# Kernel optimization log

Measured on AMD Instinct MI355X. Metric: run time of the kernel, lower is better.

## Reference

```python
import jax, jax.numpy as jnp
import numpy as np

LN_EPS = 1e-5   # torch LayerNorm default
NRM_EPS = 1e-8  # normalizer-state epsilon in mLSTMCell


def setup_inputs() -> dict:
    key = jax.random.key(0)
    ks = jax.random.split(key, 3)
    B, T, H, L, O = 32, 256, 1024, 4, 256
    x = jax.random.normal(ks[0], (B, T, H), dtype=jnp.float32)
    # 6 projections per layer in order (q, k, v, i, f, o); Linear stored as [in, out]
    W = jax.random.normal(ks[1], (L, 6, H, H), dtype=jnp.float32) * 0.02
    b = jnp.zeros((L, 6, H), dtype=jnp.float32)
    ln_g = jnp.ones((L, 6, H), dtype=jnp.float32)
    ln_b = jnp.zeros((L, 6, H), dtype=jnp.float32)
    fc_w = jax.random.normal(ks[2], (H, O), dtype=jnp.float32) * 0.02
    fc_b = jnp.zeros((O,), dtype=jnp.float32)
    return {"x": x, "W": W, "b": b, "ln_g": ln_g, "ln_b": ln_b,
            "fc_w": fc_w, "fc_b": fc_b}


def _layer_norm(z, g, beta):
    # z: [6, B, H]; g, beta: [6, H]
    mu = z.mean(-1, keepdims=True)
    var = z.var(-1, keepdims=True)
    return (z - mu) * jax.lax.rsqrt(var + LN_EPS) * g[:, None, :] + beta[:, None, :]


def _cell(x_in, h_prev, c_prev, n_prev, Wl, bl, gl, betal):
    # x_in: [B, H]; states: [B, H]; Wl: [6, H, H]
    z = jnp.einsum('bh,jhd->jbd', x_in, Wl) + bl[:, None, :]
    z = _layer_norm(z, gl, betal)
    q, k, v, zi, zf, zo = z  # q is computed by the original cell but unused
    i = jnp.exp(zi)
    f = jax.nn.sigmoid(zf)
    o = jax.nn.sigmoid(zo)
    # kv_interaction = outer(k, v); sum over dim=1 == sum(k) * v (same math, no [B,H,H])
    kv_sum = k.sum(-1, keepdims=True) * v
    c = f * c_prev + i * kv_sum
    n = f * n_prev + i * k
    n_hat = n / (jnp.linalg.norm(n, axis=-1, keepdims=True) + NRM_EPS)
    h = o * jnp.tanh(c * n_hat)
    return h, c, n


def _mlstm_forward(x, W, b, ln_g, ln_b, fc_w, fc_b):
    B, T, H = x.shape
    L = W.shape[0]
    h0 = jnp.zeros((L, B, H), x.dtype)
    init = (h0, h0, h0)  # (h, c, n)

    def step(carry, x_t):
        h, c, n = carry
        layer_in = x_t
        hs, cs, ns = [], [], []
        for l in range(L):  # small fixed layer count
            h_l, c_l, n_l = _cell(layer_in, h[l], c[l], n[l],
                                  W[l], b[l], ln_g[l], ln_b[l])
            if l > 0:  # residual connection (use_residual=True)
                h_l = h_l + layer_in
            layer_in = h_l
            hs.append(h_l); cs.append(c_l); ns.append(n_l)
        return (jnp.stack(hs), jnp.stack(cs), jnp.stack(ns)), None

    (h, c, n), _ = jax.lax.scan(step, init, jnp.swapaxes(x, 0, 1))
    # output[-1] == top-layer hidden at the final timestep
    out = h[-1] @ fc_w + fc_b  # [B, O]
    return out, (h, c, n)


def reference(x, W, b, ln_g, ln_b, fc_w, fc_b):
    return _mlstm_forward(x, W, b, ln_g, ln_b, fc_w, fc_b)
```

## Files before the change

kernel.cpp:

```cpp
#include <hip/hip_runtime.h>
#include <hip/hip_bf16.h>
#include <math.h>

#define H 1024
#define B 32
#define T 256
#define L 4
#define O 256
#define SEGLEN 16
#define NSEG (T / SEGLEN)

typedef _Float16 half8 __attribute__((ext_vector_type(8)));
typedef _Float16 half4 __attribute__((ext_vector_type(4)));
typedef float f32x4 __attribute__((ext_vector_type(4)));

#define X_PK_OFF   0
#define HB0_OFF    8388608
#define HB1_OFF    16777216
#define WT2_OFF    25165824
#define Z16_OFF    46137344
#define SEGA_OFF   88080384
#define SEGBC_OFF  89128960
#define SEGBN_OFF  90177536
#define STATS_OFF  91226112
#define CARC_OFF   91422720
#define CARN_OFF   92471296
#define FCP_OFF    93519872

__global__ __launch_bounds__(256) void pack_wx(
    const float* __restrict__ W, const float* __restrict__ x,
    _Float16* __restrict__ Wt2, _Float16* __restrict__ x_pk) {
  __shared__ float shmem[32 * 257];
  if (blockIdx.x < 5120) {
    int tile = blockIdx.x;
    int m_idx = tile >> 8;
    int kt = (tile >> 4) & 15, ntt = tile & 15;
    int l = m_idx / 5, jj = m_idx % 5;
    const float* Wf = W + ((size_t)(l * 6 + jj + 1) << 20);
    _Float16* out = Wt2 + ((size_t)m_idx << 20);
    float (*ts)[65] = (float(*)[65])shmem;
    int k0 = kt * 64, n0 = ntt * 64;
#pragma unroll
    for (int s = 0; s < 16; ++s) {
      int e = threadIdx.x + s * 256;
      int kk = e >> 6, col = e & 63;
      ts[kk][col] = Wf[(size_t)(k0 + kk) * H + n0 + col];
    }
    __syncthreads();
#pragma unroll
    for (int gi = 0; gi < 2; ++gi) {
      int g = threadIdx.x * 2 + gi;
      int l64 = g & 63, ksl = (g >> 6) & 1, ntl = g >> 7;
      int nn = l64 & 15, kh = l64 >> 4;
      half8 tmp;
#pragma unroll
      for (int e = 0; e < 8; ++e)
        tmp[e] = (_Float16)ts[ksl * 32 + kh * 8 + e][ntl * 16 + nn];
      *(half8*)&out[(size_t)((ntt * 4 + ntl) * 32 + kt * 2 + ksl) * 512 +
                    (size_t)l64 * 8] = tmp;
    }
  } else {
    int t = blockIdx.x - 5120;
    float (*ld)[257] = (float(*)[257])shmem;
    for (int c = 0; c < 4; ++c) {
      if (c) __syncthreads();
#pragma unroll
      for (int s = 0; s < 32; ++s) {
        int e2 = threadIdx.x + s * 256;
        int b = e2 >> 8, col = e2 & 255;
        ld[b][col] = x[((size_t)b * T + t) * H + c * 256 + col];
      }
      __syncthreads();
#pragma unroll
      for (int s3 = 0; s3 < 4; ++s3) {
        int gg = threadIdx.x * 4 + s3;
        int l64 = gg & 63, ksl = (gg >> 6) & 7, bt = gg >> 9;
        int nn = l64 & 15, kh = l64 >> 4;
        int b = bt * 16 + nn;
        half8 tmp;
#pragma unroll
        for (int e = 0; e < 8; ++e)
          tmp[e] = (_Float16)ld[b][ksl * 32 + kh * 8 + e];
        *(half8*)&x_pk[(size_t)t * 32768 + (size_t)bt * 16384 +
                       (size_t)(c * 8 + ksl) * 512 + (size_t)l64 * 8] = tmp;
      }
    }
  }
}

__global__ __launch_bounds__(512) void gemm_big(
    const _Float16* __restrict__ A_pk, const _Float16* __restrict__ Wl,
    _Float16* __restrict__ z16) {
  int raw = blockIdx.x;
  int xcd = raw & 7, c = raw >> 3;
  int bm = (xcd >> 1) * 16 + (c & 15);
  int bn = (xcd & 1) * 10 + (c >> 4);
  int w = threadIdx.x >> 6, lane = threadIdx.x & 63;
  int wm = w >> 2, wn = w & 3;

  __shared__ _Float16 smem[24576];

  int j = bn >> 2;
  const _Float16* gsrc[3];
  int ldst[3];
#pragma unroll
  for (int q = 0; q < 3; ++q) {
    int f = w * 3 + q;
    if (f < 8) {
      gsrc[q] = A_pk + (size_t)(bm * 8 + f) * 16384 + lane * 8;
      ldst[q] = f * 512 + lane * 8;
    } else {
      int nf = f - 8;
      gsrc[q] = Wl + ((size_t)j << 20) + (size_t)((bn & 3) * 16 + nf) * 16384 + lane * 8;
      ldst[q] = 4096 + nf * 512 + lane * 8;
    }
  }

  half8 stA[3], stB[3];
#pragma unroll
  for (int q = 0; q < 3; ++q) stA[q] = *(const half8*)(gsrc[q]);
#pragma unroll
  for (int q = 0; q < 3; ++q) *(half8*)&smem[ldst[q]] = stA[q];
#pragma unroll
  for (int q = 0; q < 3; ++q) stA[q] = *(const half8*)(gsrc[q] + 512);
  __syncthreads();

  f32x4 acc[4][4] = {};
  int ardo = wm * 2048 + lane * 8;
  int brdo = 4096 + wn * 2048 + lane * 8;

  for (int ks = 0; ks < 32; ks += 2) {
    {
      if (ks + 2 < 32) {
#pragma unroll
        for (int q = 0; q < 3; ++q)
          stB[q] = *(const half8*)(gsrc[q] + (size_t)(ks + 2) * 512);
      }
      half8 a[4], b[4];
#pragma unroll
      for (int i = 0; i < 4; ++i) a[i] = *(const half8*)&smem[ardo + i * 512];
#pragma unroll
      for (int i = 0; i < 4; ++i) b[i] = *(const half8*)&smem[brdo + i * 512];
#pragma unroll
      for (int i = 0; i < 4; ++i)
#pragma unroll
        for (int jf = 0; jf < 4; ++jf)
          acc[i][jf] = __builtin_amdgcn_mfma_f32_16x16x32_f16(a[i], b[jf], acc[i][jf], 0, 0, 0);
#pragma unroll
      for (int q = 0; q < 3; ++q) *(half8*)&smem[12288 + ldst[q]] = stA[q];
      asm volatile("s_waitcnt lgkmcnt(0)" ::: "memory");
      __builtin_amdgcn_s_barrier();
      __builtin_amdgcn_sched_barrier(0);
    }
    {
      if (ks + 3 < 32) {
#pragma unroll
        for (int q = 0; q < 3; ++q)
          stA[q] = *(const half8*)(gsrc[q] + (size_t)(ks + 3) * 512);
      }
      half8 a[4], b[4];
#pragma unroll
      for (int i = 0; i < 4; ++i) a[i] = *(const half8*)&smem[12288 + ardo + i * 512];
#pragma unroll
      for (int i = 0; i < 4; ++i) b[i] = *(const half8*)&smem[12288 + brdo + i * 512];
#pragma unroll
      for (int i = 0; i < 4; ++i)
#pragma unroll
        for (int jf = 0; jf < 4; ++jf)
          acc[i][jf] = __builtin_amdgcn_mfma_f32_16x16x32_f16(a[i], b[jf], acc[i][jf], 0, 0, 0);
      if (ks + 2 < 32) {
#pragma unroll
        for (int q = 0; q < 3; ++q) *(half8*)&smem[ldst[q]] = stB[q];
        asm volatile("s_waitcnt lgkmcnt(0)" ::: "memory");
        __builtin_amdgcn_s_barrier();
        __builtin_amdgcn_sched_barrier(0);
      }
    }
  }
  __syncthreads();

  _Float16 (*cz)[264] = (_Float16(*)[264])smem;
  int hb0 = (bn & 3) * 256;
  for (int p = 0; p < 2; ++p) {
    if (p) __syncthreads();
    if (wm == p) {
#pragma unroll
      for (int i = 0; i < 4; ++i)
#pragma unroll
        for (int jf = 0; jf < 4; ++jf)
#pragma unroll
          for (int r = 0; r < 4; ++r)
            cz[i * 16 + (lane >> 4) * 4 + r][wn * 64 + jf * 16 + (lane & 15)] =
                (_Float16)acc[i][jf][r];
    }
    __syncthreads();
#pragma unroll
    for (int s = 0; s < 4; ++s) {
      int e = threadIdx.x + s * 512;
      int r = e >> 5, h8 = e & 31;
      int m_local = bm * 128 + p * 64 + r;
      half8 vv = *(const half8*)&cz[r][h8 * 8];
      *(half8*)&z16[((size_t)m_local * 5 + j) * 1024 + hb0 + h8 * 8] = vv;
    }
  }
}

__global__ __launch_bounds__(256) void stats_kernel(
    const _Float16* __restrict__ z16, const float* __restrict__ bias,
    const float* __restrict__ ln_g, const float* __restrict__ ln_b,
    float* __restrict__ stats, int l) {
  int row = blockIdx.x, tid = threadIdx.x;
  int h0 = tid * 4;
  float red[13];
#pragma unroll
  for (int jj = 0; jj < 5; ++jj) {
    half4 z4 = *(const half4*)&z16[((size_t)row * 5 + jj) * 1024 + h0];
    float4 bb = *(const float4*)&bias[(size_t)(l * 6 + 1 + jj) * H + h0];
    float vx = (float)z4[0] + bb.x, vy = (float)z4[1] + bb.y,
          vz = (float)z4[2] + bb.z, vw = (float)z4[3] + bb.w;
    red[jj * 2] = vx + vy + vz + vw;
    red[jj * 2 + 1] = vx * vx + vy * vy + vz * vz + vw * vw;
    if (jj == 0) {
      float4 g = *(const float4*)&ln_g[(size_t)(l * 6 + 1) * H + h0];
      float4 be = *(const float4*)&ln_b[(size_t)(l * 6 + 1) * H + h0];
      red[10] = vx * g.x + vy * g.y + vz * g.z + vw * g.w;
      red[11] = g.x + g.y + g.z + g.w;
      red[12] = be.x + be.y + be.z + be.w;
    }
  }
#pragma unroll
  for (int off = 32; off; off >>= 1)
#pragma unroll
    for (int q = 0; q < 13; ++q) red[q] += __shfl_down(red[q], off);
  __shared__ float sb[4][13];
  if ((tid & 63) == 0) {
#pragma unroll
    for (int q = 0; q < 13; ++q) sb[tid >> 6][q] = red[q];
  }
  __syncthreads();
  if (tid == 0) {
    float st[13];
#pragma unroll
    for (int q = 0; q < 13; ++q) st[q] = sb[0][q] + sb[1][q] + sb[2][q] + sb[3][q];
    float* so = stats + (size_t)row * 12;
#pragma unroll
    for (int jj = 0; jj < 5; ++jj) {
      float mu = st[jj * 2] * (1.0f / H);
      float var = st[jj * 2 + 1] * (1.0f / H) - mu * mu;
      so[jj * 2] = mu;
      so[jj * 2 + 1] = rsqrtf(var + 1e-5f);
    }
    float mu0 = st[0] * (1.0f / H);
    float rs0 = rsqrtf(st[1] * (1.0f / H) - mu0 * mu0 + 1e-5f);
    so[10] = rs0 * (st[10] - mu0 * st[11]) + st[12];
    so[11] = 0.f;
  }
}

__global__ __launch_bounds__(256) void scan_p1agg(
    const _Float16* __restrict__ z16, const float* __restrict__ stats,
    const float* __restrict__ bias, const float* __restrict__ ln_g,
    const float* __restrict__ ln_b, float* __restrict__ segA,
    float* __restrict__ segBc, float* __restrict__ segBn, int l) {
  int idx = blockIdx.x * 256 + threadIdx.x;
  int h = idx & 1023;
  int bs = idx >> 10;
  int b = bs & 31, seg = bs >> 5;

  float bz[4], gg[4], bb[4];
#pragma unroll
  for (int jj = 0; jj < 4; ++jj) {
    bz[jj] = bias[(size_t)(l * 6 + 1 + jj) * H + h];
    gg[jj] = ln_g[(size_t)(l * 6 + 1 + jj) * H + h];
    bb[jj] = ln_b[(size_t)(l * 6 + 1 + jj) * H + h];
  }
  float A = 1.f, bc = 0.f, bn = 0.f;
#pragma unroll 2
  for (int u = 0; u < SEGLEN; ++u) {
    int row = (seg * SEGLEN + u) * 32 + b;
    size_t zb = ((size_t)row * 5) * 1024 + h;
    float zk = (float)z16[zb];
    float zv = (float)z16[zb + 1024];
    float zi = (float)z16[zb + 2048];
    float zf = (float)z16[zb + 3072];
    const float* st = stats + (size_t)row * 12;
    float k   = (zk + bz[0] - st[0]) * st[1] * gg[0] + bb[0];
    float v   = (zv + bz[1] - st[2]) * st[3] * gg[1] + bb[1];
    float zi_ = (zi + bz[2] - st[4]) * st[5] * gg[2] + bb[2];
    float zf_ = (zf + bz[3] - st[6]) * st[7] * gg[3] + bb[3];
    float iv = __expf(zi_);
    float fv = 1.f / (1.f + __expf(-zf_));
    A *= fv;
    bn = fv * bn + iv * k;
    bc = fv * bc + iv * (st[10] * v);
  }
  size_t so = ((size_t)seg * 32 + b) * 1024 + h;
  segA[so] = A;
  segBn[so] = bn;
  segBc[so] = bc;
}

__global__ __launch_bounds__(256) void scan_p2(
    const float* __restrict__ segA, const float* __restrict__ segBc,
    const float* __restrict__ segBn, float* __restrict__ carC,
    float* __restrict__ carN) {
  int idx = blockIdx.x * 256 + threadIdx.x;
  int h = idx & 1023, b = idx >> 10;
  float cc = 0.f, nn = 0.f;
#pragma unroll
  for (int seg = 0; seg < NSEG; ++seg) {
    size_t coff = (size_t)seg * 32768 + (size_t)b * 1024 + h;
    carC[coff] = cc;
    carN[coff] = nn;
    size_t so = ((size_t)seg * 32 + b) * 1024 + h;
    float a = segA[so];
    cc = segBc[so] + a * cc;
    nn = segBn[so] + a * nn;
  }
}

__global__ __launch_bounds__(256) void final_scan(
    const _Float16* __restrict__ z16, const float* __restrict__ stats,
    const float* __restrict__ bias, const float* __restrict__ ln_g,
    const float* __restrict__ ln_b, const float* __restrict__ carC,
    const float* __restrict__ carN, const _Float16* __restrict__ hin,
    _Float16* __restrict__ hout, float* __restrict__ out, int l) {
  int seg = blockIdx.x >> 5, b = blockIdx.x & 31;
  int tid = threadIdx.x, h0 = tid * 4;

  float bz[5][4], gg[5][4], bb[5][4];
#pragma unroll
  for (int jj = 0; jj < 5; ++jj) {
    float4 t1 = *(const float4*)&bias[(size_t)(l * 6 + 1 + jj) * H + h0];
    float4 t2 = *(const float4*)&ln_g[(size_t)(l * 6 + 1 + jj) * H + h0];
    float4 t3 = *(const float4*)&ln_b[(size_t)(l * 6 + 1 + jj) * H + h0];
    bz[jj][0] = t1.x; bz[jj][1] = t1.y; bz[jj][2] = t1.z; bz[jj][3] = t1.w;
    gg[jj][0] = t2.x; gg[jj][1] = t2.y; gg[jj][2] = t2.z; gg[jj][3] = t2.w;
    bb[jj][0] = t3.x; bb[jj][1] = t3.y; bb[jj][2] = t3.z; bb[jj][3] = t3.w;
  }

  size_t coff = (size_t)seg * 32768 + (size_t)b * 1024 + h0;
  float4 cC4 = *(const float4*)&carC[coff];
  float4 cN4 = *(const float4*)&carN[coff];
  float c_[4] = {cC4.x, cC4.y, cC4.z, cC4.w};
  float n_[4] = {cN4.x, cN4.y, cN4.z, cN4.w};

  size_t hfoff = (size_t)(b >> 4) * 16384 + (size_t)(h0 >> 5) * 512 +
                 (size_t)((((h0 & 31) >> 3) * 16) + (b & 15)) * 8 + (h0 & 7);
  __shared__ float sbuf[2][4];

  half4 zr[5];
  {
    int row0 = (seg * SEGLEN) * 32 + b;
#pragma unroll
    for (int jj = 0; jj < 5; ++jj)
      zr[jj] = *(const half4*)&z16[((size_t)row0 * 5 + jj) * 1024 + h0];
  }

  for (int u = 0; u < SEGLEN; ++u) {
    int t = seg * SEGLEN + u;
    int row = t * 32 + b;
    half4 zc[5];
#pragma unroll
    for (int jj = 0; jj < 5; ++jj) zc[jj] = zr[jj];
    if (u + 1 < SEGLEN) {
      int rown = (t + 1) * 32 + b;
#pragma unroll
      for (int jj = 0; jj < 5; ++jj)
        zr[jj] = *(const half4*)&z16[((size_t)rown * 5 + jj) * 1024 + h0];
    }
    half4 rin;
    if (l > 0) rin = *(const half4*)&hin[(size_t)t * 32768 + hfoff];

    const float* st = stats + (size_t)row * 12;
    float mu0 = st[0], rs0 = st[1], mu1 = st[2], rs1 = st[3];
    float mu2 = st[4], rs2 = st[5], mu3 = st[6], rs3 = st[7];
    float mu4 = st[8], rs4 = st[9], ksum = st[10];

    float ss = 0.f;
#pragma unroll
    for (int e = 0; e < 4; ++e) {
      float k   = ((float)zc[0][e] + bz[0][e] - mu0) * rs0 * gg[0][e] + bb[0][e];
      float v   = ((float)zc[1][e] + bz[1][e] - mu1) * rs1 * gg[1][e] + bb[1][e];
      float zi_ = ((float)zc[2][e] + bz[2][e] - mu2) * rs2 * gg[2][e] + bb[2][e];
      float zf_ = ((float)zc[3][e] + bz[3][e] - mu3) * rs3 * gg[3][e] + bb[3][e];
      float iv = __expf(zi_);
      float fv = 1.f / (1.f + __expf(-zf_));
      n_[e] = fv * n_[e] + iv * k;
      c_[e] = fv * c_[e] + iv * (ksum * v);
      ss += n_[e] * n_[e];
    }
#pragma unroll
    for (int off = 32; off; off >>= 1) ss += __shfl_down(ss, off);
    if ((tid & 63) == 0) sbuf[u & 1][tid >> 6] = ss;
    __syncthreads();
    float nrm = sbuf[u & 1][0] + sbuf[u & 1][1] + sbuf[u & 1][2] + sbuf[u & 1][3];
    float rn = 1.f / (sqrtf(nrm) + 1e-8f);

    float hh[4];
#pragma unroll
    for (int e = 0; e < 4; ++e) {
      float zo_ = ((float)zc[4][e] + bz[4][e] - mu4) * rs4 * gg[4][e] + bb[4][e];
      float ov = 1.f / (1.f + __expf(-zo_));
      float targ = c_[e] * (n_[e] * rn);
      float e2 = __expf(-2.f * fabsf(targ));
      float th = copysignf((1.f - e2) / (1.f + e2), targ);
      hh[e] = ov * th + ((l > 0) ? (float)rin[e] : 0.f);
    }
    half4 hx;
    hx[0] = (_Float16)hh[0]; hx[1] = (_Float16)hh[1];
    hx[2] = (_Float16)hh[2]; hx[3] = (_Float16)hh[3];
    *(half4*)&hout[(size_t)t * 32768 + hfoff] = hx;

    if (t == T - 1) {
      *(float4*)&out[8192 + (size_t)l * 32768 + (size_t)b * 1024 + h0] =
          make_float4(hh[0], hh[1], hh[2], hh[3]);
      *(float4*)&out[8192 + 131072 + ((size_t)(l * B) + b) * 1024 + h0] =
          make_float4(c_[0], c_[1], c_[2], c_[3]);
      *(float4*)&out[8192 + 262144 + ((size_t)(l * B) + b) * 1024 + h0] =
          make_float4(n_[0], n_[1], n_[2], n_[3]);
    }
  }
}

__global__ __launch_bounds__(256) void fc_part(
    const float* __restrict__ out_h, const float* __restrict__ fc_w,
    float* __restrict__ partial) {
  int b = blockIdx.x >> 3, kh = blockIdx.x & 7;
  int o = threadIdx.x;
  const float* hr = out_h + (size_t)b * 1024 + kh * 128;
  const float* wp = fc_w + (size_t)kh * 128 * O + o;
  float acc = 0.f;
#pragma unroll 8
  for (int h = 0; h < 128; ++h)
    acc = fmaf(hr[h], wp[(size_t)h * O], acc);
  partial[((size_t)kh * 32 + b) * O + o] = acc;
}

__global__ __launch_bounds__(256) void fc_reduce(
    const float* __restrict__ partial, const float* __restrict__ fc_b,
    float* __restrict__ out) {
  int b = blockIdx.x, o = threadIdx.x;
  float acc = fc_b[o];
#pragma unroll
  for (int kh = 0; kh < 8; ++kh)
    acc += partial[((size_t)kh * 32 + b) * O + o];
  out[(size_t)b * O + o] = acc;
}

extern "C" void kernel_launch(void* const* d_in, const int* in_sizes, int n_in,
                              void* d_out, int out_size, void* d_ws, size_t ws_size,
                              hipStream_t stream) {
  const float* x    = (const float*)d_in[0];
  const float* W    = (const float*)d_in[1];
  const float* bias = (const float*)d_in[2];
  const float* ln_g = (const float*)d_in[3];
  const float* ln_b = (const float*)d_in[4];
  const float* fc_w = (const float*)d_in[5];
  const float* fc_b = (const float*)d_in[6];
  float* out = (float*)d_out;
  _Float16* wsh = (_Float16*)d_ws;

  _Float16* x_pk = wsh + X_PK_OFF;
  _Float16* hb[2] = {wsh + HB0_OFF, wsh + HB1_OFF};
  _Float16* Wt2  = wsh + WT2_OFF;
  _Float16* z16  = wsh + Z16_OFF;
  float* segA  = (float*)(wsh + SEGA_OFF);
  float* segBc = (float*)(wsh + SEGBC_OFF);
  float* segBn = (float*)(wsh + SEGBN_OFF);
  float* stats = (float*)(wsh + STATS_OFF);
  float* carC  = (float*)(wsh + CARC_OFF);
  float* carN  = (float*)(wsh + CARN_OFF);
  float* fcp   = (float*)(wsh + FCP_OFF);

  pack_wx<<<5376, 256, 0, stream>>>(W, x, Wt2, x_pk);

  for (int l = 0; l < L; ++l) {
    const _Float16* A_in = (l == 0) ? x_pk : hb[(l - 1) & 1];
    _Float16* h_out = hb[l & 1];
    const _Float16* Wl = Wt2 + ((size_t)(l * 5) << 20);
    gemm_big<<<1280, 512, 0, stream>>>(A_in, Wl, z16);
    stats_kernel<<<8192, 256, 0, stream>>>(z16, bias, ln_g, ln_b, stats, l);
    scan_p1agg<<<2048, 256, 0, stream>>>(z16, stats, bias, ln_g, ln_b,
                                         segA, segBc, segBn, l);
    scan_p2<<<128, 256, 0, stream>>>(segA, segBc, segBn, carC, carN);
    final_scan<<<512, 256, 0, stream>>>(z16, stats, bias, ln_g, ln_b,
                                        carC, carN, A_in, h_out, out, l);
  }
  fc_part<<<256, 256, 0, stream>>>(out + 8192 + 3 * 32768, fc_w, fcp);
  fc_reduce<<<B, 256, 0, stream>>>(fcp, fc_b, out);
}
```

Before: 759.0 us.

## Enlarge GEMM tile to 256 rows with direct global-to-LDS async loads

The main per-layer GEMM now computes a 256x256 output tile per block instead of 128x256, halving the grid to 640 blocks and doubling reuse of each loaded weight tile. Operand staging switches from register round-trips to global_load_lds direct-to-LDS copies. It uses a 128 KB dynamic shared-memory double buffer with a 64-wide K step. This is meant to cut global traffic and VGPR staging overhead. The cost is one block per CU with fewer waves to hide latency, and possibly worse tail balance across CUs.

```diff
diff --git a/kernel.cpp b/kernel.cpp
--- a/kernel.cpp
+++ b/kernel.cpp
@@ -26,6 +26,12 @@
 #define CARC_OFF   91422720
 #define CARN_OFF   92471296
 #define FCP_OFF    93519872
+
+__device__ __forceinline__ void gll16(const _Float16* g, _Float16* l) {
+  __builtin_amdgcn_global_load_lds(
+      (const __attribute__((address_space(1))) void*)g,
+      (__attribute__((address_space(3))) void*)l, 16, 0, 0);
+}
 
 __global__ __launch_bounds__(256) void pack_wx(
     const float* __restrict__ W, const float* __restrict__ x,
@@ -88,117 +94,106 @@
   }
 }
 
-__global__ __launch_bounds__(512) void gemm_big(
+extern "C" __global__ __launch_bounds__(512, 1) void gemm_big(
     const _Float16* __restrict__ A_pk, const _Float16* __restrict__ Wl,
     _Float16* __restrict__ z16) {
+  extern __shared__ _Float16 smem[];
   int raw = blockIdx.x;
   int xcd = raw & 7, c = raw >> 3;
-  int bm = (xcd >> 1) * 16 + (c & 15);
-  int bn = (xcd & 1) * 10 + (c >> 4);
+  int bm = (xcd >> 1) * 8 + (c & 7);
+  int bn = (xcd & 1) * 10 + (c >> 3);
   int w = threadIdx.x >> 6, lane = threadIdx.x & 63;
   int wm = w >> 2, wn = w & 3;
-
-  __shared__ _Float16 smem[24576];
-
   int j = bn >> 2;
-  const _Float16* gsrc[3];
-  int ldst[3];
-#pragma unroll
-  for (int q = 0; q < 3; ++q) {
-    int f = w * 3 + q;
-    if (f < 8) {
-      gsrc[q] = A_pk + (size_t)(bm * 8 + f) * 16384 + lane * 8;
-      ldst[q] = f * 512 + lane * 8;
+
+  const _Float16* gbase[8];
+  int lbase[8];
+#pragma unroll
+  for (int q = 0; q < 8; ++q) {
+    int f = w * 8 + q;
+    if (f < 32) {
+      int rm = f >> 1, ks2 = f & 1;
+      gbase[q] = A_pk + (size_t)(bm * 16 + rm) * 16384 + (size_t)ks2 * 512 + lane * 8;
+      lbase[q] = (rm * 2 + ks2) * 512;
     } else {
-      int nf = f - 8;
-      gsrc[q] = Wl + ((size_t)j << 20) + (size_t)((bn & 3) * 16 + nf) * 16384 + lane * 8;
-      ldst[q] = 4096 + nf * 512 + lane * 8;
-    }
-  }
-
-  half8 stA[3], stB[3];
-#pragma unroll
-  for (int q = 0; q < 3; ++q) stA[q] = *(const half8*)(gsrc[q]);
-#pragma unroll
-  for (int q = 0; q < 3; ++q) *(half8*)&smem[ldst[q]] = stA[q];
-#pragma unroll
-  for (int q = 0; q < 3; ++q) stA[q] = *(const half8*)(gsrc[q] + 512);
-  __syncthreads();
-
-  f32x4 acc[4][4] = {};
-  int ardo = wm * 2048 + lane * 8;
-  int brdo = 4096 + wn * 2048 + lane * 8;
-
-  for (int ks = 0; ks < 32; ks += 2) {
-    {
-      if (ks + 2 < 32) {
-#pragma unroll
-        for (int q = 0; q < 3; ++q)
-          stB[q] = *(const half8*)(gsrc[q] + (size_t)(ks + 2) * 512);
+      int f2 = f - 32;
+      int ntl = f2 >> 1, ks2 = f2 & 1;
+      gbase[q] = Wl + ((size_t)j << 20) + (size_t)((bn & 3) * 16 + ntl) * 16384 +
+                 (size_t)ks2 * 512 + lane * 8;
+      lbase[q] = 16384 + (ntl * 2 + ks2) * 512;
+    }
+  }
+
+#pragma unroll
+  for (int q = 0; q < 8; ++q) gll16(gbase[q], &smem[lbase[q]]);
+  asm volatile("s_waitcnt vmcnt(0)" ::: "memory");
+  __builtin_amdgcn_s_barrier();
+  __builtin_amdgcn_sched_barrier(0);
+
+  f32x4 acc[8][4] = {};
+  int abase = wm * 8 * 1024;
+  int bbase = 16384 + wn * 4 * 1024;
+
+  for (int kt = 0; kt < 16; ++kt) {
+    int cur = (kt & 1) * 32768;
+    int nxt = cur ^ 32768;
+    half8 b[4][2];
+#pragma unroll
+    for (int jf = 0; jf < 4; ++jf)
+#pragma unroll
+      for (int k2 = 0; k2 < 2; ++k2)
+        b[jf][k2] = *(const half8*)&smem[cur + bbase + (jf * 2 + k2) * 512 + lane * 8];
+#pragma unroll
+    for (int p = 0; p < 4; ++p) {
+      if (p < 2 && kt + 1 < 16) {
+#pragma unroll
+        for (int q = 0; q < 4; ++q)
+          gll16(gbase[p * 4 + q] + (size_t)(kt + 1) * 1024,
+                &smem[nxt + lbase[p * 4 + q]]);
       }
-      half8 a[4], b[4];
-#pragma unroll
-      for (int i = 0; i < 4; ++i) a[i] = *(const half8*)&smem[ardo + i * 512];
-#pragma unroll
-      for (int i = 0; i < 4; ++i) b[i] = *(const half8*)&smem[brdo + i * 512];
-#pragma unroll
-      for (int i = 0; i < 4; ++i)
+      half8 a[2][2];
+#pragma unroll
+      for (int i2 = 0; i2 < 2; ++i2)
+#pragma unroll
+        for (int k2 = 0; k2 < 2; ++k2)
+          a[i2][k2] = *(const half8*)&smem[cur + abase + ((p * 2 + i2) * 2 + k2) * 512 + lane * 8];
+#pragma unroll
+      for (int i2 = 0; i2 < 2; ++i2)
 #pragma unroll
         for (int jf = 0; jf < 4; ++jf)
-          acc[i][jf] = __builtin_amdgcn_mfma_f32_16x16x32_f16(a[i], b[jf], acc[i][jf], 0, 0, 0);
-#pragma unroll
-      for (int q = 0; q < 3; ++q) *(half8*)&smem[12288 + ldst[q]] = stA[q];
-      asm volatile("s_waitcnt lgkmcnt(0)" ::: "memory");
-      __builtin_amdgcn_s_barrier();
-      __builtin_amdgcn_sched_barrier(0);
-    }
-    {
-      if (ks + 3 < 32) {
-#pragma unroll
-        for (int q = 0; q < 3; ++q)
-          stA[q] = *(const half8*)(gsrc[q] + (size_t)(ks + 3) * 512);
-      }
-      half8 a[4], b[4];
-#pragma unroll
-      for (int i = 0; i < 4; ++i) a[i] = *(const half8*)&smem[12288 + ardo + i * 512];
-#pragma unroll
-      for (int i = 0; i < 4; ++i) b[i] = *(const half8*)&smem[12288 + brdo + i * 512];
-#pragma unroll
-      for (int i = 0; i < 4; ++i)
-#pragma unroll
-        for (int jf = 0; jf < 4; ++jf)
-          acc[i][jf] = __builtin_amdgcn_mfma_f32_16x16x32_f16(a[i], b[jf], acc[i][jf], 0, 0, 0);
-      if (ks + 2 < 32) {
-#pragma unroll
-        for (int q = 0; q < 3; ++q) *(half8*)&smem[ldst[q]] = stB[q];
-        asm volatile("s_waitcnt lgkmcnt(0)" ::: "memory");
-        __builtin_amdgcn_s_barrier();
-        __builtin_amdgcn_sched_barrier(0);
-      }
-    }
+#pragma unroll
+          for (int k2 = 0; k2 < 2; ++k2)
+            acc[p * 2 + i2][jf] = __builtin_amdgcn_mfma_f32_16x16x32_f16(
+                a[i2][k2], b[jf][k2], acc[p * 2 + i2][jf], 0, 0, 0);
+    }
+    asm volatile("s_waitcnt vmcnt(0) lgkmcnt(0)" ::: "memory");
+    __builtin_amdgcn_s_barrier();
+    __builtin_amdgcn_sched_barrier(0);
   }
   __syncthreads();
 
   _Float16 (*cz)[264] = (_Float16(*)[264])smem;
   int hb0 = (bn & 3) * 256;
-  for (int p = 0; p < 2; ++p) {
-    if (p) __syncthreads();
-    if (wm == p) {
-#pragma unroll
-      for (int i = 0; i < 4; ++i)
+  for (int g = 0; g < 4; ++g) {
+    if (g) __syncthreads();
+    if (wm == (g >> 1)) {
+#pragma unroll
+      for (int r4 = 0; r4 < 4; ++r4) {
+        int fi = (g & 1) * 4 + r4;
 #pragma unroll
         for (int jf = 0; jf < 4; ++jf)
 #pragma unroll
           for (int r = 0; r < 4; ++r)
-            cz[i * 16 + (lane >> 4) * 4 + r][wn * 64 + jf * 16 + (lane & 15)] =
-                (_Float16)acc[i][jf][r];
+            cz[r4 * 16 + (lane >> 4) * 4 + r][wn * 64 + jf * 16 + (lane & 15)] =
+                (_Float16)acc[fi][jf][r];
+      }
     }
     __syncthreads();
 #pragma unroll
     for (int s = 0; s < 4; ++s) {
       int e = threadIdx.x + s * 512;
       int r = e >> 5, h8 = e & 31;
-      int m_local = bm * 128 + p * 64 + r;
+      int m_local = bm * 256 + g * 64 + r;
       half8 vv = *(const half8*)&cz[r][h8 * 8];
       *(half8*)&z16[((size_t)m_local * 5 + j) * 1024 + hb0 + h8 * 8] = vv;
     }
@@ -473,13 +468,20 @@
   float* carN  = (float*)(wsh + CARN_OFF);
   float* fcp   = (float*)(wsh + FCP_OFF);
 
+  static bool attr_set = false;
+  if (!attr_set) {
+    (void)hipFuncSetAttribute((const void*)gemm_big,
+                              hipFuncAttributeMaxDynamicSharedMemorySize, 131072);
+    attr_set = true;
+  }
+
   pack_wx<<<5376, 256, 0, stream>>>(W, x, Wt2, x_pk);
 
   for (int l = 0; l < L; ++l) {
     const _Float16* A_in = (l == 0) ? x_pk : hb[(l - 1) & 1];
     _Float16* h_out = hb[l & 1];
     const _Float16* Wl = Wt2 + ((size_t)(l * 5) << 20);
-    gemm_big<<<1280, 512, 0, stream>>>(A_in, Wl, z16);
+    gemm_big<<<640, 512, 131072, stream>>>(A_in, Wl, z16);
     stats_kernel<<<8192, 256, 0, stream>>>(z16, bias, ln_g, ln_b, stats, l);
     scan_p1agg<<<2048, 256, 0, stream>>>(z16, stats, bias, ln_g, ln_b,
                                          segA, segBc, segBn, l);
```

Result: slower. 795.8 us (+4.9%).
